# Kernel optimization log

Measured on AMD Instinct MI355X. Metric: run time of the kernel, lower is better.

## Reference

```python
import jax, jax.numpy as jnp
import numpy as np

B, N, NC, D, H = 2, 8192, 512, 512, 16
HD = D // H            # 32
SCALE = HD ** -0.5
EPS = 1e-6


def setup_inputs() -> dict:
    key = jax.random.key(0)
    k0, k1, k2, k3, k4 = jax.random.split(key, 5)
    return {
        "x": jax.random.normal(k0, (B, N, D), dtype=jnp.float32),
        "clusters": jax.random.normal(k1, (B, NC, D), dtype=jnp.float32),
        "Wq": jax.random.normal(k2, (D, D), dtype=jnp.float32) * 0.02,
        "Wkv": jax.random.normal(k3, (D, 2 * D), dtype=jnp.float32) * 0.02,
        "Wout": jax.random.normal(k4, (D, D), dtype=jnp.float32) * 0.02,
    }


def reference(x, clusters, Wq, Wkv, Wout):
    # projections (torch Linear without bias == matmul with weight)
    q = clusters @ Wq                      # [b, nc, d]
    kv = x @ Wkv                           # [b, n, 2d]
    # split heads: 'b n (h d) -> b h n d' and 'b n (k h d) -> k b h n d'
    q = q.reshape(B, NC, H, HD).transpose(0, 2, 1, 3)        # [b, h, nc, hd]
    kv = kv.reshape(B, N, 2, H, HD)
    k = kv[:, :, 0].transpose(0, 2, 1, 3)                    # [b, h, n, hd]
    v = kv[:, :, 1].transpose(0, 2, 1, 3)                    # [b, h, n, hd]

    attn = jnp.einsum('bhqd,bhkd->bhqk', q, k) * SCALE       # [b, h, nc, n]
    # 'soft' assignment: softmax over the CLUSTER (query) axis, dim=-2
    attn = jax.nn.softmax(attn, axis=-2)
    token_sizes = attn.sum(-1)                               # [b, h, nc]
    attn = attn / (token_sizes[..., None] + EPS)
    token_sizes = token_sizes.mean(axis=1)                   # [b, nc]

    out = jnp.einsum('bhqk,bhkd->bhqd', attn, v)             # [b, h, nc, hd]
    out = out.transpose(0, 2, 1, 3).reshape(B, NC, D)        # [b, nc, d]
    out = out @ Wout
    return out, token_sizes
```

## Files before the change

kernel.cpp:

```cpp
#include <hip/hip_runtime.h>
#include <hip/hip_bf16.h>

#define B_ 2
#define N_ 8192
#define NC_ 512
#define D_ 512
#define H_ 16
#define HD_ 32
#define SCALE_ 0.17677669529663687f
#define EPS_ 1e-6f
#define NCHUNK 16
#define CHUNK (N_ / NCHUNK)

typedef __attribute__((ext_vector_type(8))) short bf16x8_t;
typedef __attribute__((ext_vector_type(4))) short bf16x4_t;
typedef __attribute__((ext_vector_type(4))) float f32x4_t;

static __device__ __forceinline__ short f2bf(float f) {
    unsigned u = __float_as_uint(f);
    unsigned r = (u + 0x7FFFu + ((u >> 16) & 1u)) >> 16;
    return (short)r;
}

static __device__ __forceinline__ void gload_lds16(const short* g, void* l) {
    __builtin_amdgcn_global_load_lds(
        (const __attribute__((address_space(1))) void*)g,
        (__attribute__((address_space(3))) void*)l, 16, 0, 0);
}

__global__ __launch_bounds__(256) void cvt_bf16_kernel(
    const float* __restrict__ a, short* __restrict__ ao, int na8,
    const float* __restrict__ b, short* __restrict__ bo)
{
    int i8 = blockIdx.x * 256 + threadIdx.x;
    const float* src; short* dst;
    if (i8 < na8) { src = a + (size_t)i8 * 8; dst = ao + (size_t)i8 * 8; }
    else { size_t o = (size_t)(i8 - na8) * 8; src = b + o; dst = bo + o; }
    float4 v0 = *(const float4*)src;
    float4 v1 = *(const float4*)(src + 4);
    bf16x8_t p = {f2bf(v0.x), f2bf(v0.y), f2bf(v0.z), f2bf(v0.w),
                  f2bf(v1.x), f2bf(v1.y), f2bf(v1.z), f2bf(v1.w)};
    *(bf16x8_t*)dst = p;
}

__global__ __launch_bounds__(256) void transpose_cvt_kernel(
    const float* __restrict__ Wq, const float* __restrict__ Wkv,
    const float* __restrict__ Wout,
    short* __restrict__ WqT, short* __restrict__ WkvT, short* __restrict__ WoutT)
{
    const float* src; short* dst; int ncols;
    if (blockIdx.z == 0)      { src = Wq;   dst = WqT;   ncols = 512; }
    else if (blockIdx.z == 1) { src = Wkv;  dst = WkvT;  ncols = 1024; }
    else                      { src = Wout; dst = WoutT; ncols = 512; }
    if ((int)blockIdx.x * 32 >= ncols) return;

    __shared__ short t[32][34];
    const int c0 = blockIdx.x * 32, r0 = blockIdx.y * 32;
    const int tc = threadIdx.x & 31, tr = threadIdx.x >> 5;
#pragma unroll
    for (int i = 0; i < 4; i++) {
        int r = tr + i * 8;
        t[tc][r] = f2bf(src[(size_t)(r0 + r) * ncols + c0 + tc]);
    }
    __syncthreads();
#pragma unroll
    for (int i = 0; i < 4; i++) {
        int outr = tr + i * 8;
        dst[(size_t)(c0 + outr) * 512 + r0 + tc] = t[outr][tc];
    }
}

template <bool OUT_BF16>
__global__ __launch_bounds__(256) void gemm_bt_kernel(
    const short* __restrict__ A, const short* __restrict__ BT,
    void* __restrict__ C, int M, int N, int K)
{
    __shared__ short As[128 * 32];
    __shared__ short Bs[128 * 32];

    const int tid = threadIdx.x;
    const int wid = tid >> 6, lane = tid & 63;
    const int l16 = lane & 15, lg = lane >> 4;
    const int wr = (wid >> 1) * 64, wc = (wid & 1) * 64;

    const int nwg = gridDim.x * gridDim.y;
    const int flat = blockIdx.y * gridDim.x + blockIdx.x;
    const int swz = (flat & 7) * (nwg >> 3) + (flat >> 3);
    const int bx = swz % gridDim.x, by = swz / gridDim.x;

    const f32x4_t zero4 = {0.f, 0.f, 0.f, 0.f};
    f32x4_t acc[4][4];
#pragma unroll
    for (int i = 0; i < 4; i++)
#pragma unroll
        for (int j = 0; j < 4; j++) acc[i][j] = zero4;

    const short* aptr = A + (size_t)(by * 128 + wid * 16 + (lane >> 2)) * K + (lane & 3) * 8;
    const short* bptr = BT + (size_t)(bx * 128 + wid * 16 + (lane >> 2)) * K + (lane & 3) * 8;
    char* al = (char*)As + wid * 1024;
    char* bl = (char*)Bs + wid * 1024;
    const size_t rstep = (size_t)64 * K;

    for (int kt = 0; kt < K; kt += 32) {
        gload_lds16(aptr + kt, al);
        gload_lds16(aptr + rstep + kt, al + 4096);
        gload_lds16(bptr + kt, bl);
        gload_lds16(bptr + rstep + kt, bl + 4096);
        __syncthreads();

        bf16x8_t bfr[4];
#pragma unroll
        for (int nf = 0; nf < 4; nf++)
            bfr[nf] = *(const bf16x8_t*)&Bs[(wc + nf * 16 + l16) * 32 + lg * 8];
#pragma unroll
        for (int mf = 0; mf < 4; mf++) {
            bf16x8_t afr = *(const bf16x8_t*)&As[(wr + mf * 16 + l16) * 32 + lg * 8];
#pragma unroll
            for (int nf = 0; nf < 4; nf++)
                acc[mf][nf] = __builtin_amdgcn_mfma_f32_16x16x32_bf16(
                    afr, bfr[nf], acc[mf][nf], 0, 0, 0);
        }
        __syncthreads();
    }

#pragma unroll
    for (int mf = 0; mf < 4; mf++) {
#pragma unroll
        for (int nf = 0; nf < 4; nf++) {
            int row0 = by * 128 + wr + mf * 16 + lg * 4;
            int col  = bx * 128 + wc + nf * 16 + l16;
#pragma unroll
            for (int r = 0; r < 4; r++) {
                float v = acc[mf][nf][r];
                if (OUT_BF16)
                    ((short*)C)[(size_t)(row0 + r) * N + col] = f2bf(v);
                else
                    ((float*)C)[(size_t)(row0 + r) * N + col] = v;
            }
        }
    }
}

__global__ __launch_bounds__(256) void attn_kernel(
    const short* __restrict__ qb,
    const short* __restrict__ kvb,
    float* __restrict__ out_part,
    float* __restrict__ ts_part)
{
    const int chunk = blockIdx.x, h = blockIdx.y, b = blockIdx.z;
    const int tid = threadIdx.x, wid = tid >> 6, lane = tid & 63;
    const int l16 = lane & 15, lg = lane >> 4;

    __shared__ short P_lds[512][40];
    __shared__ short v_t[32][40];
    __shared__ float reds[2][4][16];

    bf16x8_t qf[8];
#pragma unroll
    for (int mf = 0; mf < 8; mf++) {
        int row = wid * 128 + mf * 16 + l16;
        qf[mf] = *(const bf16x8_t*)&qb[(size_t)(b * NC_ + row) * D_ + h * HD_ + lg * 8];
    }

    const f32x4_t zero4 = {0.f, 0.f, 0.f, 0.f};
    f32x4_t oacc[8][2], tsacc[8];
#pragma unroll
    for (int mf = 0; mf < 8; mf++) {
        oacc[mf][0] = zero4; oacc[mf][1] = zero4; tsacc[mf] = zero4;
    }
    bf16x8_t onesf;
#pragma unroll
    for (int j = 0; j < 8; j++) onesf[j] = (short)0x3F80;

    const int kchunk0 = chunk * CHUNK;

    for (int kt = 0; kt < CHUNK / 32; kt++) {
        const int kb = kchunk0 + kt * 32;
        __syncthreads();
        {
            int key = tid >> 3, d0 = (tid & 7) * 4;
            bf16x4_t vv = *(const bf16x4_t*)&kvb[(size_t)(b * N_ + kb + key) * (2 * D_) + D_ + h * HD_ + d0];
            v_t[d0 + 0][key] = vv[0];
            v_t[d0 + 1][key] = vv[1];
            v_t[d0 + 2][key] = vv[2];
            v_t[d0 + 3][key] = vv[3];
        }
#pragma unroll
        for (int half = 0; half < 2; half++) {
            const int kc = half * 16;
            bf16x8_t kf = *(const bf16x8_t*)&kvb[(size_t)(b * N_ + kb + kc + l16) * (2 * D_) + h * HD_ + lg * 8];
            f32x4_t sacc[8];
#pragma unroll
            for (int mf = 0; mf < 8; mf++)
                sacc[mf] = __builtin_amdgcn_mfma_f32_16x16x32_bf16(qf[mf], kf, zero4, 0, 0, 0);

            float sloc = 0.f;
#pragma unroll
            for (int mf = 0; mf < 8; mf++)
#pragma unroll
                for (int r = 0; r < 4; r++) {
                    float e = __expf(sacc[mf][r] * SCALE_);
                    sacc[mf][r] = e;
                    sloc += e;
                }
            sloc += __shfl_xor(sloc, 16, 64);
            sloc += __shfl_xor(sloc, 32, 64);
            if (lane < 16) reds[half][wid][lane] = sloc;
            __syncthreads();
            float inv = 1.f / (reds[half][0][l16] + reds[half][1][l16] +
                               reds[half][2][l16] + reds[half][3][l16]);

#pragma unroll
            for (int mf = 0; mf < 8; mf++)
#pragma unroll
                for (int r = 0; r < 4; r++)
                    P_lds[wid * 128 + mf * 16 + lg * 4 + r][kc + l16] =
                        f2bf(sacc[mf][r] * inv);
        }

        bf16x8_t v0 = *(const bf16x8_t*)&v_t[l16][lg * 8];
        bf16x8_t v1 = *(const bf16x8_t*)&v_t[16 + l16][lg * 8];
#pragma unroll
        for (int mf = 0; mf < 8; mf++) {
            bf16x8_t pa = *(const bf16x8_t*)&P_lds[wid * 128 + mf * 16 + l16][lg * 8];
            oacc[mf][0] = __builtin_amdgcn_mfma_f32_16x16x32_bf16(pa, v0, oacc[mf][0], 0, 0, 0);
            oacc[mf][1] = __builtin_amdgcn_mfma_f32_16x16x32_bf16(pa, v1, oacc[mf][1], 0, 0, 0);
            tsacc[mf]   = __builtin_amdgcn_mfma_f32_16x16x32_bf16(pa, onesf, tsacc[mf], 0, 0, 0);
        }
    }

    const size_t base = ((size_t)(chunk * B_ + b) * H_ + h);
#pragma unroll
    for (int mf = 0; mf < 8; mf++) {
        int row0 = wid * 128 + mf * 16 + lg * 4;
#pragma unroll
        for (int nf = 0; nf < 2; nf++) {
            int col = nf * 16 + l16;
#pragma unroll
            for (int r = 0; r < 4; r++)
                out_part[(base * NC_ + row0 + r) * HD_ + col] = oacc[mf][nf][r];
        }
        if (l16 == 0) {
#pragma unroll
            for (int r = 0; r < 4; r++)
                ts_part[base * NC_ + row0 + r] = tsacc[mf][r];
        }
    }
}

__global__ __launch_bounds__(256) void reduce_kernel(
    const float* __restrict__ out_part, const float* __restrict__ ts_part,
    short* __restrict__ out_mid, float* __restrict__ tok_out)
{
    const int bnc = blockIdx.x;
    const int b = bnc >> 9, nc = bnc & 511;
    const int t = threadIdx.x;
    __shared__ float tsh[16];
    if (t < 16) {
        float s = 0.f;
#pragma unroll
        for (int ch = 0; ch < NCHUNK; ch++)
            s += ts_part[((size_t)(ch * B_ + b) * H_ + t) * NC_ + nc];
        tsh[t] = s;
    }
    __syncthreads();
    if (t == 0) {
        float s = 0.f;
#pragma unroll
        for (int i = 0; i < 16; i++) s += tsh[i];
        tok_out[b * NC_ + nc] = s * (1.f / 16.f);
    }
    for (int c = t; c < D_; c += 256) {
        int hh = c >> 5, d = c & 31;
        float s = 0.f;
#pragma unroll
        for (int ch = 0; ch < NCHUNK; ch++)
            s += out_part[(((size_t)(ch * B_ + b) * H_ + hh) * NC_ + nc) * HD_ + d];
        out_mid[(size_t)(b * NC_ + nc) * D_ + c] = f2bf(s / (tsh[hh] + EPS_));
    }
}

extern "C" void kernel_launch(void* const* d_in, const int* in_sizes, int n_in,
                              void* d_out, int out_size, void* d_ws, size_t ws_size,
                              hipStream_t stream)
{
    (void)in_sizes; (void)n_in; (void)out_size; (void)ws_size;
    const float* x        = (const float*)d_in[0];
    const float* clusters = (const float*)d_in[1];
    const float* Wq       = (const float*)d_in[2];
    const float* Wkv      = (const float*)d_in[3];
    const float* Wout     = (const float*)d_in[4];

    char* ws = (char*)d_ws;
    short* x_bf     = (short*)(ws);
    short* WkvT     = (short*)(ws + 16777216);
    short* cl_bf    = (short*)(ws + 17825792);
    short* WqT      = (short*)(ws + 18874368);
    float* out_part = (float*)(ws);
    float* ts_part  = (float*)(ws + 33554432);
    short* kvb      = (short*)(ws + 34603008);
    short* qb       = (short*)(ws + 68157440);
    short* WoutT    = (short*)(ws + 69206016);
    short* out_mid  = (short*)(ws + 69730304);

    float* out = (float*)d_out;
    float* tok = out + (size_t)B_ * NC_ * D_;

    cvt_bf16_kernel<<<dim3(4352), dim3(256), 0, stream>>>(
        x, x_bf, (B_ * N_ * D_) / 8, clusters, cl_bf);
    transpose_cvt_kernel<<<dim3(32, 16, 3), dim3(256), 0, stream>>>(
        Wq, Wkv, Wout, WqT, WkvT, WoutT);
    gemm_bt_kernel<true><<<dim3((2 * D_) / 128, (B_ * N_) / 128), dim3(256), 0, stream>>>(
        x_bf, WkvT, kvb, B_ * N_, 2 * D_, D_);
    gemm_bt_kernel<true><<<dim3(D_ / 128, (B_ * NC_) / 128), dim3(256), 0, stream>>>(
        cl_bf, WqT, qb, B_ * NC_, D_, D_);
    attn_kernel<<<dim3(NCHUNK, H_, B_), dim3(256), 0, stream>>>(
        qb, kvb, out_part, ts_part);
    reduce_kernel<<<dim3(B_ * NC_), dim3(256), 0, stream>>>(
        out_part, ts_part, out_mid, tok);
    gemm_bt_kernel<false><<<dim3(D_ / 128, (B_ * NC_) / 128), dim3(256), 0, stream>>>(
        out_mid, WoutT, d_out, B_ * NC_, D_, D_);
}
```

Before: 137.3 us.

## Double attention chunks, fold scale into Q, swizzle P in LDS, bf16 partials

Doubles the number of key chunks in the attention kernel so more blocks run in parallel, and sets launch bounds aiming for four blocks per CU. The softmax scale and log2(e) are folded into the Q projection epilogue so exp2f can be used. Both 16-key halves are now computed before a single barrier, P uses an XOR-swizzled unpadded LDS layout with truncating bf16 conversion, and the partial outputs are written as bf16 to halve reduce traffic. Workspace offsets are rearranged to fit. The cost is lower precision in P and in the partial sums, plus twice as many partials for the reduce kernel to sum.

Result: slower. 316.9 us (+130.8%).

```diff
diff --git a/kernel.cpp b/kernel.cpp
--- a/kernel.cpp
+++ b/kernel.cpp
@@ -8,8 +8,9 @@
 #define H_ 16
 #define HD_ 32
 #define SCALE_ 0.17677669529663687f
+#define LOG2E_ 1.4426950408889634f
 #define EPS_ 1e-6f
-#define NCHUNK 16
+#define NCHUNK 32
 #define CHUNK (N_ / NCHUNK)
 
 typedef __attribute__((ext_vector_type(8))) short bf16x8_t;
@@ -73,7 +74,7 @@
 template <bool OUT_BF16>
 __global__ __launch_bounds__(256) void gemm_bt_kernel(
     const short* __restrict__ A, const short* __restrict__ BT,
-    void* __restrict__ C, int M, int N, int K)
+    void* __restrict__ C, int M, int N, int K, float oscale)
 {
     __shared__ short As[128 * 32];
     __shared__ short Bs[128 * 32];
@@ -131,7 +132,7 @@
             int col  = bx * 128 + wc + nf * 16 + l16;
 #pragma unroll
             for (int r = 0; r < 4; r++) {
-                float v = acc[mf][nf][r];
+                float v = acc[mf][nf][r] * oscale;
                 if (OUT_BF16)
                     ((short*)C)[(size_t)(row0 + r) * N + col] = f2bf(v);
                 else
@@ -141,17 +142,17 @@
     }
 }
 
-__global__ __launch_bounds__(256) void attn_kernel(
+__global__ __launch_bounds__(256, 4) void attn_kernel(
     const short* __restrict__ qb,
     const short* __restrict__ kvb,
-    float* __restrict__ out_part,
+    short* __restrict__ out_part,
     float* __restrict__ ts_part)
 {
     const int chunk = blockIdx.x, h = blockIdx.y, b = blockIdx.z;
     const int tid = threadIdx.x, wid = tid >> 6, lane = tid & 63;
     const int l16 = lane & 15, lg = lane >> 4;
 
-    __shared__ short P_lds[512][40];
+    __shared__ short P_lds[512 * 32];
     __shared__ short v_t[32][40];
     __shared__ float reds[2][4][16];
 
@@ -172,57 +173,78 @@
 #pragma unroll
     for (int j = 0; j < 8; j++) onesf[j] = (short)0x3F80;
 
-    const int kchunk0 = chunk * CHUNK;
+    const short* kptr = kvb + (size_t)(b * N_ + chunk * CHUNK + l16) * (2 * D_) + h * HD_ + lg * 8;
+    const int skey = tid >> 3, sd0 = (tid & 7) * 4;
+    const short* vptr = kvb + (size_t)(b * N_ + chunk * CHUNK + skey) * (2 * D_) + D_ + h * HD_ + sd0;
+    char* Pb = (char*)P_lds;
 
     for (int kt = 0; kt < CHUNK / 32; kt++) {
-        const int kb = kchunk0 + kt * 32;
+        const size_t koff = (size_t)kt * 32 * (2 * D_);
         __syncthreads();
         {
-            int key = tid >> 3, d0 = (tid & 7) * 4;
-            bf16x4_t vv = *(const bf16x4_t*)&kvb[(size_t)(b * N_ + kb + key) * (2 * D_) + D_ + h * HD_ + d0];
-            v_t[d0 + 0][key] = vv[0];
-            v_t[d0 + 1][key] = vv[1];
-            v_t[d0 + 2][key] = vv[2];
-            v_t[d0 + 3][key] = vv[3];
-        }
-#pragma unroll
-        for (int half = 0; half < 2; half++) {
-            const int kc = half * 16;
-            bf16x8_t kf = *(const bf16x8_t*)&kvb[(size_t)(b * N_ + kb + kc + l16) * (2 * D_) + h * HD_ + lg * 8];
-            f32x4_t sacc[8];
-#pragma unroll
-            for (int mf = 0; mf < 8; mf++)
-                sacc[mf] = __builtin_amdgcn_mfma_f32_16x16x32_bf16(qf[mf], kf, zero4, 0, 0, 0);
-
-            float sloc = 0.f;
-#pragma unroll
-            for (int mf = 0; mf < 8; mf++)
-#pragma unroll
-                for (int r = 0; r < 4; r++) {
-                    float e = __expf(sacc[mf][r] * SCALE_);
-                    sacc[mf][r] = e;
-                    sloc += e;
-                }
-            sloc += __shfl_xor(sloc, 16, 64);
-            sloc += __shfl_xor(sloc, 32, 64);
-            if (lane < 16) reds[half][wid][lane] = sloc;
-            __syncthreads();
-            float inv = 1.f / (reds[half][0][l16] + reds[half][1][l16] +
-                               reds[half][2][l16] + reds[half][3][l16]);
-
-#pragma unroll
-            for (int mf = 0; mf < 8; mf++)
-#pragma unroll
-                for (int r = 0; r < 4; r++)
-                    P_lds[wid * 128 + mf * 16 + lg * 4 + r][kc + l16] =
-                        f2bf(sacc[mf][r] * inv);
+            bf16x4_t vv = *(const bf16x4_t*)(vptr + koff);
+            v_t[sd0 + 0][skey] = vv[0];
+            v_t[sd0 + 1][skey] = vv[1];
+            v_t[sd0 + 2][skey] = vv[2];
+            v_t[sd0 + 3][skey] = vv[3];
+        }
+        bf16x8_t kf0 = *(const bf16x8_t*)(kptr + koff);
+        bf16x8_t kf1 = *(const bf16x8_t*)(kptr + koff + 16 * (2 * D_));
+        f32x4_t s0[8], s1[8];
+#pragma unroll
+        for (int mf = 0; mf < 8; mf++)
+            s0[mf] = __builtin_amdgcn_mfma_f32_16x16x32_bf16(qf[mf], kf0, zero4, 0, 0, 0);
+#pragma unroll
+        for (int mf = 0; mf < 8; mf++)
+            s1[mf] = __builtin_amdgcn_mfma_f32_16x16x32_bf16(qf[mf], kf1, zero4, 0, 0, 0);
+
+        float sl0 = 0.f, sl1 = 0.f;
+#pragma unroll
+        for (int mf = 0; mf < 8; mf++)
+#pragma unroll
+            for (int r = 0; r < 4; r++) {
+                float e = exp2f(s0[mf][r]);
+                s0[mf][r] = e; sl0 += e;
+            }
+#pragma unroll
+        for (int mf = 0; mf < 8; mf++)
+#pragma unroll
+            for (int r = 0; r < 4; r++) {
+                float e = exp2f(s1[mf][r]);
+                s1[mf][r] = e; sl1 += e;
+            }
+        sl0 += __shfl_xor(sl0, 16, 64); sl0 += __shfl_xor(sl0, 32, 64);
+        sl1 += __shfl_xor(sl1, 16, 64); sl1 += __shfl_xor(sl1, 32, 64);
+        if (lane < 16) reds[0][wid][lane] = sl0;
+        else if (lane < 32) reds[1][wid][lane - 16] = sl1;
+        __syncthreads();
+
+        float inv0 = __fdividef(1.f, reds[0][0][l16] + reds[0][1][l16] +
+                                     reds[0][2][l16] + reds[0][3][l16]);
+        float inv1 = __fdividef(1.f, reds[1][0][l16] + reds[1][1][l16] +
+                                     reds[1][2][l16] + reds[1][3][l16]);
+
+#pragma unroll
+        for (int mf = 0; mf < 8; mf++) {
+#pragma unroll
+            for (int r = 0; r < 4; r++) {
+                int row = wid * 128 + mf * 16 + lg * 4 + r;
+                int x = (row >> 1) & 3;
+                int by0 = row * 64 + ((l16 & 7) * 2) + ((((l16 >> 3) ^ x) & 3) << 4);
+                *(short*)(Pb + by0) = (short)(__float_as_uint(s0[mf][r] * inv0) >> 16);
+                int k1 = 16 + l16;
+                int by1 = row * 64 + ((k1 & 7) * 2) + ((((k1 >> 3) ^ x) & 3) << 4);
+                *(short*)(Pb + by1) = (short)(__float_as_uint(s1[mf][r] * inv1) >> 16);
+            }
         }
 
         bf16x8_t v0 = *(const bf16x8_t*)&v_t[l16][lg * 8];
         bf16x8_t v1 = *(const bf16x8_t*)&v_t[16 + l16][lg * 8];
 #pragma unroll
         for (int mf = 0; mf < 8; mf++) {
-            bf16x8_t pa = *(const bf16x8_t*)&P_lds[wid * 128 + mf * 16 + l16][lg * 8];
+            int row = wid * 128 + mf * 16 + l16;
+            bf16x8_t pa = *(const bf16x8_t*)(Pb + row * 64 +
+                              (((lg ^ ((row >> 1) & 3)) & 3) << 4));
             oacc[mf][0] = __builtin_amdgcn_mfma_f32_16x16x32_bf16(pa, v0, oacc[mf][0], 0, 0, 0);
             oacc[mf][1] = __builtin_amdgcn_mfma_f32_16x16x32_bf16(pa, v1, oacc[mf][1], 0, 0, 0);
             tsacc[mf]   = __builtin_amdgcn_mfma_f32_16x16x32_bf16(pa, onesf, tsacc[mf], 0, 0, 0);
@@ -238,7 +260,7 @@
             int col = nf * 16 + l16;
 #pragma unroll
             for (int r = 0; r < 4; r++)
-                out_part[(base * NC_ + row0 + r) * HD_ + col] = oacc[mf][nf][r];
+                out_part[(base * NC_ + row0 + r) * HD_ + col] = f2bf(oacc[mf][nf][r]);
         }
         if (l16 == 0) {
 #pragma unroll
@@ -249,7 +271,7 @@
 }
 
 __global__ __launch_bounds__(256) void reduce_kernel(
-    const float* __restrict__ out_part, const float* __restrict__ ts_part,
+    const short* __restrict__ out_part, const float* __restrict__ ts_part,
     short* __restrict__ out_mid, float* __restrict__ tok_out)
 {
     const int bnc = blockIdx.x;
@@ -274,8 +296,11 @@
         int hh = c >> 5, d = c & 31;
         float s = 0.f;
 #pragma unroll
-        for (int ch = 0; ch < NCHUNK; ch++)
-            s += out_part[(((size_t)(ch * B_ + b) * H_ + hh) * NC_ + nc) * HD_ + d];
+        for (int ch = 0; ch < NCHUNK; ch++) {
+            unsigned short u = (unsigned short)
+                out_part[(((size_t)(ch * B_ + b) * H_ + hh) * NC_ + nc) * HD_ + d];
+            s += __uint_as_float((unsigned)u << 16);
+        }
         out_mid[(size_t)(b * NC_ + nc) * D_ + c] = f2bf(s / (tsh[hh] + EPS_));
     }
 }
@@ -296,12 +321,12 @@
     short* WkvT     = (short*)(ws + 16777216);
     short* cl_bf    = (short*)(ws + 17825792);
     short* WqT      = (short*)(ws + 18874368);
-    float* out_part = (float*)(ws);
+    short* out_part = (short*)(ws);
     float* ts_part  = (float*)(ws + 33554432);
-    short* kvb      = (short*)(ws + 34603008);
-    short* qb       = (short*)(ws + 68157440);
-    short* WoutT    = (short*)(ws + 69206016);
-    short* out_mid  = (short*)(ws + 69730304);
+    short* kvb      = (short*)(ws + 35651584);
+    short* out_mid  = (short*)(ws + 35651584);
+    short* qb       = (short*)(ws + 69206016);
+    short* WoutT    = (short*)(ws + 70254592);
 
     float* out = (float*)d_out;
     float* tok = out + (size_t)B_ * NC_ * D_;
@@ -311,13 +336,13 @@
     transpose_cvt_kernel<<<dim3(32, 16, 3), dim3(256), 0, stream>>>(
         Wq, Wkv, Wout, WqT, WkvT, WoutT);
     gemm_bt_kernel<true><<<dim3((2 * D_) / 128, (B_ * N_) / 128), dim3(256), 0, stream>>>(
-        x_bf, WkvT, kvb, B_ * N_, 2 * D_, D_);
+        x_bf, WkvT, kvb, B_ * N_, 2 * D_, D_, 1.0f);
     gemm_bt_kernel<true><<<dim3(D_ / 128, (B_ * NC_) / 128), dim3(256), 0, stream>>>(
-        cl_bf, WqT, qb, B_ * NC_, D_, D_);
+        cl_bf, WqT, qb, B_ * NC_, D_, D_, SCALE_ * LOG2E_);
     attn_kernel<<<dim3(NCHUNK, H_, B_), dim3(256), 0, stream>>>(
         qb, kvb, out_part, ts_part);
     reduce_kernel<<<dim3(B_ * NC_), dim3(256), 0, stream>>>(
         out_part, ts_part, out_mid, tok);
     gemm_bt_kernel<false><<<dim3(D_ / 128, (B_ * NC_) / 128), dim3(256), 0, stream>>>(
-        out_mid, WoutT, d_out, B_ * NC_, D_, D_);
-}
+        out_mid, WoutT, d_out, B_ * NC_, D_, D_, 1.0f);
+}
```
